# Performance work log

Measured on AMD Instinct MI355X. Metric: run time of the kernel, lower is better.

The kernel has to match this reference:

```python
import jax, jax.numpy as jnp
import numpy as np

HID = 128
HEADS = 4
CH = HID // HEADS          # 32
EDGE_DIM = 2 * HID         # H_update mode
GROUPS = 8
NEG_SLOPE = 0.2
EPS_GN = 1e-5
EPS_LN = 1e-5
N_NODES = 32768
N_EDGES = 524288


def setup_inputs() -> dict:
    key = jax.random.key(0)
    ks = jax.random.split(key, 32)
    N, E, C = N_NODES, N_EDGES, HID
    s = lambda fan: 1.0 / np.sqrt(fan)
    inp = dict(
        h_target=jax.random.normal(ks[0], (N, C), jnp.float32),
        h_source=jax.random.normal(ks[1], (N, C), jnp.float32),
        pos=jax.random.normal(ks[2], (N, 2), jnp.float32),
        t_emb=jax.random.normal(ks[3], (N, C), jnp.float32),
        edge_index=jax.random.randint(ks[4], (2, E), 0, N, jnp.int32),
        # AdaGN params
        gn_gamma=jnp.ones((C,), jnp.float32),
        gn_beta=jnp.zeros((C,), jnp.float32),
        fc_W=jax.random.normal(ks[5], (C, 2 * C), jnp.float32) * s(C),
        fc_b=jnp.zeros((2 * C,), jnp.float32),
        # GATv2 params
        Wl=jax.random.normal(ks[6], (C, HEADS * CH), jnp.float32) * s(C),
        bl=jnp.zeros((HEADS * CH,), jnp.float32),
        Wr=jax.random.normal(ks[7], (C, HEADS * CH), jnp.float32) * s(C),
        br=jnp.zeros((HEADS * CH,), jnp.float32),
        We=jax.random.normal(ks[8], (EDGE_DIM, HEADS * CH), jnp.float32) * s(EDGE_DIM),
        att=jax.random.normal(ks[9], (HEADS, CH), jnp.float32) * s(CH),
        gat_bias=jnp.zeros((HEADS * CH,), jnp.float32),
        # post GAT linear
        Wpost=jax.random.normal(ks[10], (C, C), jnp.float32) * s(C),
        bpost=jnp.zeros((C,), jnp.float32),
        # update MLP: LayerNorm -> Linear -> GELU -> Linear
        ln_g=jnp.ones((C,), jnp.float32),
        ln_b=jnp.zeros((C,), jnp.float32),
        W1=jax.random.normal(ks[11], (C, C), jnp.float32) * s(C),
        b1=jnp.zeros((C,), jnp.float32),
        W2=jax.random.normal(ks[12], (C, C), jnp.float32) * s(C),
        b2=jnp.zeros((C,), jnp.float32),
    )
    return inp


def _adagn(x, cond, gn_gamma, gn_beta, fc_W, fc_b):
    N, C = x.shape
    xg = x.reshape(N, GROUPS, C // GROUPS)
    mu = xg.mean(-1, keepdims=True)
    var = xg.var(-1, keepdims=True)
    normed = ((xg - mu) * jax.lax.rsqrt(var + EPS_GN)).reshape(N, C)
    normed = normed * gn_gamma + gn_beta
    style = cond @ fc_W + fc_b
    gamma, beta = jnp.split(style, 2, axis=-1)
    return normed * (1.0 + gamma) + beta


def reference(h_target, h_source, pos, t_emb, edge_index,
              gn_gamma, gn_beta, fc_W, fc_b,
              Wl, bl, Wr, br, We, att, gat_bias,
              Wpost, bpost, ln_g, ln_b, W1, b1, W2, b2):
    N, C = h_source.shape
    src, dst = edge_index[0], edge_index[1]

    h_src_mod = _adagn(h_source, t_emb, gn_gamma, gn_beta, fc_W, fc_b)

    # physics edge features (H_update mode)
    d_vec = pos[src] - pos[dst]                       # [E,2]
    dx, dy = d_vec[:, 0:1], d_vec[:, 1:2]
    dist_sq = jnp.maximum((d_vec ** 2).sum(-1, keepdims=True), 1e-8)
    grad_mag = (h_src_mod[src] - h_src_mod[dst]) / dist_sq   # [E,C]
    edge_attr = jnp.concatenate([grad_mag * (-dy), grad_mag * dx], axis=-1)  # [E,2C]

    # GATv2Conv (eval mode, no dropout)
    xl = (h_src_mod @ Wl + bl).reshape(N, HEADS, CH)  # source transform
    xr = (h_src_mod @ Wr + br).reshape(N, HEADS, CH)  # target transform
    e = (edge_attr @ We).reshape(-1, HEADS, CH)
    z = jax.nn.leaky_relu(xl[src] + xr[dst] + e, NEG_SLOPE)   # [E,H,Ch]
    logit = jnp.einsum('ehc,hc->eh', z, att)                  # [E,H]
    m = jax.ops.segment_max(logit, dst, num_segments=N)       # [N,H]
    m = jnp.where(jnp.isfinite(m), m, 0.0)
    ex = jnp.exp(logit - m[dst])
    denom = jax.ops.segment_sum(ex, dst, num_segments=N)      # [N,H]
    alpha = ex / (denom[dst] + 1e-16)                         # [E,H]
    msg = xl[src] * alpha[..., None]                          # [E,H,Ch]
    aggr = jax.ops.segment_sum(msg, dst, num_segments=N).reshape(N, HEADS * CH)
    aggr = aggr + gat_bias

    aggr = aggr @ Wpost + bpost

    # update MLP with residual
    mu = aggr.mean(-1, keepdims=True)
    var = aggr.var(-1, keepdims=True)
    ln = (aggr - mu) * jax.lax.rsqrt(var + EPS_LN) * ln_g + ln_b
    h = jax.nn.gelu(ln @ W1 + b1, approximate=False) @ W2 + b2
    return h_target + h
```

## Files before the change

### kernel.cpp

```cpp
#include <hip/hip_runtime.h>
#include <hip/hip_bf16.h>
#include <math.h>

#define HID 128

typedef __bf16 bf16x8 __attribute__((ext_vector_type(8)));
typedef float f32x4 __attribute__((ext_vector_type(4)));
union BF8 { uint4 u; bf16x8 v; unsigned short s[8]; };

__device__ __forceinline__ unsigned short f2bf(float x) {
  unsigned u = __float_as_uint(x);
  unsigned r = u + 0x7FFFu + ((u >> 16) & 1u);
  return (unsigned short)(r >> 16);
}
__device__ __forceinline__ float bf2f(unsigned short h) {
  return __uint_as_float(((unsigned)h) << 16);
}
__device__ __forceinline__ void ld2bf(const unsigned short* p, float& x, float& y) {
  unsigned v = *(const unsigned*)p;
  x = __uint_as_float((v & 0xFFFFu) << 16);
  y = __uint_as_float(v & 0xFFFF0000u);
}

__global__ void prep3(const float* __restrict__ fc_W, const float* __restrict__ Wl,
                      const float* __restrict__ Wr, const float* __restrict__ We,
                      const float* __restrict__ Wpost, const float* __restrict__ W1,
                      const float* __restrict__ W2, const float* __restrict__ bl,
                      const float* __restrict__ br, const float* __restrict__ gat_bias,
                      const float* __restrict__ bpost,
                      unsigned short* __restrict__ fcTh, unsigned short* __restrict__ fcTl,
                      unsigned short* __restrict__ WnTh, unsigned short* __restrict__ WnTl,
                      unsigned short* __restrict__ WpT, unsigned short* __restrict__ W1T,
                      unsigned short* __restrict__ W2T,
                      float* __restrict__ bxy, float* __restrict__ bpost2) {
  int gid = blockIdx.x * 256 + threadIdx.x;
  if (gid < 32768) {
    int n = gid >> 7, k = gid & 127;
    float x = fc_W[k * 256 + n];
    unsigned short h = f2bf(x);
    fcTh[n * 128 + k] = h;
    fcTl[n * 128 + k] = f2bf(x - bf2f(h));
  } else if (gid < 98304) {
    int i = gid - 32768; int n = i >> 7, k = i & 127;
    float x;
    if (n < 128)      x = Wl[k * 128 + n];
    else if (n < 256) x = Wr[k * 128 + (n - 128)];
    else if (n < 384) x = We[k * 128 + (n - 256)];
    else              x = We[(128 + k) * 128 + (n - 384)];
    unsigned short h = f2bf(x);
    WnTh[n * 128 + k] = h;
    if (n >= 256) WnTl[(n - 256) * 128 + k] = f2bf(x - bf2f(h));
  } else if (gid < 147456) {
    int i = gid - 98304; int which = i >> 14; int j = i & 16383;
    int n = j >> 7, k = j & 127;
    const float* W = (which == 0) ? Wpost : (which == 1) ? W1 : W2;
    unsigned short* T = (which == 0) ? WpT : (which == 1) ? W1T : W2T;
    T[n * 128 + k] = f2bf(W[k * 128 + n]);
  } else if (gid < 147712) {
    int j = gid - 147456;
    bxy[j] = (j < 128) ? bl[j] : br[j - 128];
  } else if (gid < 147840) {
    int t = gid - 147712;
    float s = bpost[t];
    for (int k = 0; k < 128; ++k) s += gat_bias[k] * Wpost[k * 128 + t];
    bpost2[t] = s;
  }
}

__global__ __launch_bounds__(256) void gemm_mfma(const float* __restrict__ A,
                                                 const unsigned short* __restrict__ WTh,
                                                 const unsigned short* __restrict__ WTl,
                                                 const float* __restrict__ bias,
                                                 float* __restrict__ C, int Ncols) {
  int tid = threadIdx.x;
  int wave = tid >> 6, lane = tid & 63;
  int m = lane & 15, q = lane >> 4;
  int r0 = blockIdx.x * 64 + wave * 16;
  const float* arow = A + (size_t)(r0 + m) * 128 + q * 8;
  BF8 Ah[4], Al[4];
#pragma unroll
  for (int kc = 0; kc < 4; ++kc) {
    float4 x0 = *(const float4*)(arow + kc * 32);
    float4 x1 = *(const float4*)(arow + kc * 32 + 4);
    float xs[8] = {x0.x, x0.y, x0.z, x0.w, x1.x, x1.y, x1.z, x1.w};
#pragma unroll
    for (int j = 0; j < 8; ++j) {
      unsigned short h = f2bf(xs[j]);
      Ah[kc].s[j] = h;
      Al[kc].s[j] = f2bf(xs[j] - bf2f(h));
    }
  }
  int ntiles = Ncols >> 4;
  for (int nt = 0; nt < ntiles; ++nt) {
    const unsigned short* wr  = WTh + (size_t)(nt * 16 + m) * 128 + q * 8;
    const unsigned short* wrl = WTl + (size_t)(nt * 16 + m) * 128 + q * 8;
    f32x4 acc = {0.f, 0.f, 0.f, 0.f};
#pragma unroll
    for (int kc = 0; kc < 4; ++kc) {
      BF8 bh, blo;
      bh.u  = *(const uint4*)(wr + kc * 32);
      blo.u = *(const uint4*)(wrl + kc * 32);
      acc = __builtin_amdgcn_mfma_f32_16x16x32_bf16(Ah[kc].v, bh.v, acc, 0, 0, 0);
      acc = __builtin_amdgcn_mfma_f32_16x16x32_bf16(Al[kc].v, bh.v, acc, 0, 0, 0);
      acc = __builtin_amdgcn_mfma_f32_16x16x32_bf16(Ah[kc].v, blo.v, acc, 0, 0, 0);
    }
    int n = nt * 16 + m;
    float bv = bias ? bias[n] : 0.0f;
#pragma unroll
    for (int i = 0; i < 4; ++i) {
      int row = r0 + q * 4 + i;
      C[(size_t)row * Ncols + n] = acc[i] + bv;
    }
  }
}

__global__ __launch_bounds__(256) void k_nodeP(const float* __restrict__ h_source,
                                               const float* __restrict__ style,
                                               const float* __restrict__ gn_gamma,
                                               const float* __restrict__ gn_beta,
                                               const unsigned short* __restrict__ WnTh,
                                               const unsigned short* __restrict__ WnTl,
                                               const float* __restrict__ bxy,
                                               unsigned short* __restrict__ packed,
                                               unsigned short* __restrict__ xrArr) {
  int tid = threadIdx.x, wave = tid >> 6, lane = tid & 63;
  int m = lane & 15, q = lane >> 4;
  int r0 = blockIdx.x * 128 + wave * 32;
  BF8 Ah[2][4], Al[2][4];
#pragma unroll
  for (int set = 0; set < 2; ++set) {
    int r = r0 + set * 16 + m;
    const float* hrow = h_source + (size_t)r * 128;
    const float* srow = style + (size_t)r * 256;
#pragma unroll
    for (int kc = 0; kc < 4; ++kc) {
      int ch = q * 8 + kc * 32;
      float4 x0 = *(const float4*)(hrow + ch);
      float4 x1 = *(const float4*)(hrow + ch + 4);
      float xs[8] = {x0.x, x0.y, x0.z, x0.w, x1.x, x1.y, x1.z, x1.w};
      float s8 = 0.f, q8 = 0.f;
#pragma unroll
      for (int j = 0; j < 8; ++j) { s8 += xs[j]; q8 += xs[j] * xs[j]; }
      float s16 = s8 + __shfl_xor(s8, 16);
      float q16 = q8 + __shfl_xor(q8, 16);
      float mu = s16 * (1.0f / 16.0f);
      float var = q16 * (1.0f / 16.0f) - mu * mu;
      float rv = rsqrtf(var + 1e-5f);
      float4 g0 = *(const float4*)(gn_gamma + ch);
      float4 g1 = *(const float4*)(gn_gamma + ch + 4);
      float4 be0 = *(const float4*)(gn_beta + ch);
      float4 be1 = *(const float4*)(gn_beta + ch + 4);
      float4 sg0 = *(const float4*)(srow + ch);
      float4 sg1 = *(const float4*)(srow + ch + 4);
      float4 sb0 = *(const float4*)(srow + 128 + ch);
      float4 sb1 = *(const float4*)(srow + 128 + ch + 4);
      float gg[8] = {g0.x, g0.y, g0.z, g0.w, g1.x, g1.y, g1.z, g1.w};
      float bb[8] = {be0.x, be0.y, be0.z, be0.w, be1.x, be1.y, be1.z, be1.w};
      float sg[8] = {sg0.x, sg0.y, sg0.z, sg0.w, sg1.x, sg1.y, sg1.z, sg1.w};
      float sb[8] = {sb0.x, sb0.y, sb0.z, sb0.w, sb1.x, sb1.y, sb1.z, sb1.w};
#pragma unroll
      for (int j = 0; j < 8; ++j) {
        float v = ((xs[j] - mu) * rv * gg[j] + bb[j]) * (1.0f + sg[j]) + sb[j];
        unsigned short h = f2bf(v);
        Ah[set][kc].s[j] = h;
        Al[set][kc].s[j] = f2bf(v - bf2f(h));
      }
    }
  }
  for (int nt = 0; nt < 32; ++nt) {
    f32x4 acc0 = {0.f, 0.f, 0.f, 0.f};
    f32x4 acc1 = {0.f, 0.f, 0.f, 0.f};
    const unsigned short* wr = WnTh + (size_t)(nt * 16 + m) * 128 + q * 8;
    if (nt < 16) {
#pragma unroll
      for (int kc = 0; kc < 4; ++kc) {
        BF8 bh; bh.u = *(const uint4*)(wr + kc * 32);
        acc0 = __builtin_amdgcn_mfma_f32_16x16x32_bf16(Ah[0][kc].v, bh.v, acc0, 0, 0, 0);
        acc1 = __builtin_amdgcn_mfma_f32_16x16x32_bf16(Ah[1][kc].v, bh.v, acc1, 0, 0, 0);
      }
    } else {
      const unsigned short* wl = WnTl + (size_t)((nt - 16) * 16 + m) * 128 + q * 8;
#pragma unroll
      for (int kc = 0; kc < 4; ++kc) {
        BF8 bh, blo;
        bh.u  = *(const uint4*)(wr + kc * 32);
        blo.u = *(const uint4*)(wl + kc * 32);
        acc0 = __builtin_amdgcn_mfma_f32_16x16x32_bf16(Ah[0][kc].v, bh.v, acc0, 0, 0, 0);
        acc0 = __builtin_amdgcn_mfma_f32_16x16x32_bf16(Al[0][kc].v, bh.v, acc0, 0, 0, 0);
        acc0 = __builtin_amdgcn_mfma_f32_16x16x32_bf16(Ah[0][kc].v, blo.v, acc0, 0, 0, 0);
        acc1 = __builtin_amdgcn_mfma_f32_16x16x32_bf16(Ah[1][kc].v, bh.v, acc1, 0, 0, 0);
        acc1 = __builtin_amdgcn_mfma_f32_16x16x32_bf16(Al[1][kc].v, bh.v, acc1, 0, 0, 0);
        acc1 = __builtin_amdgcn_mfma_f32_16x16x32_bf16(Ah[1][kc].v, blo.v, acc1, 0, 0, 0);
      }
    }
    int n = nt * 16 + m;
    float bv = (nt < 16) ? bxy[n] : 0.0f;
#pragma unroll
    for (int set = 0; set < 2; ++set) {
      f32x4 a = set ? acc1 : acc0;
#pragma unroll
      for (int i = 0; i < 4; ++i) {
        int row = r0 + set * 16 + q * 4 + i;
        unsigned short h = f2bf(a[i] + bv);
        if (nt < 8)       packed[(size_t)row * 384 + n] = h;
        else if (nt < 16) xrArr[(size_t)row * 128 + (n - 128)] = h;
        else              packed[(size_t)row * 384 + 128 + (n - 256)] = h;
      }
    }
  }
}

__global__ __launch_bounds__(256) void k_hist(const int* __restrict__ edst,
                                              int* __restrict__ count, int E) {
  int e = blockIdx.x * 256 + threadIdx.x;
  if (e < E) atomicAdd(&count[edst[e]], 1);
}

__global__ __launch_bounds__(1024) void k_scan(const int* __restrict__ count,
                                               int* __restrict__ rowptr,
                                               int* __restrict__ cursor, int N, int E) {
  __shared__ int part[1024];
  int t = threadIdx.x;
  int base = t * 32;
  int local[32];
  int s = 0;
#pragma unroll
  for (int i = 0; i < 32; ++i) { local[i] = count[base + i]; s += local[i]; }
  part[t] = s;
  __syncthreads();
  for (int off = 1; off < 1024; off <<= 1) {
    int v = part[t];
    int addv = (t >= off) ? part[t - off] : 0;
    __syncthreads();
    part[t] = v + addv;
    __syncthreads();
  }
  int run = (t == 0) ? 0 : part[t - 1];
#pragma unroll
  for (int i = 0; i < 32; ++i) {
    rowptr[base + i] = run;
    cursor[base + i] = run;
    run += local[i];
  }
  if (t == 1023) rowptr[N] = E;
}

__global__ __launch_bounds__(256) void k_scatter(const int* __restrict__ esrc,
                                                 const int* __restrict__ edst,
                                                 const float* __restrict__ pos,
                                                 int* __restrict__ cursor,
                                                 float4* __restrict__ meta, int E) {
  int e = blockIdx.x * 256 + threadIdx.x;
  if (e >= E) return;
  int src = esrc[e], dst = edst[e];
  int p = atomicAdd(&cursor[dst], 1);
  float2 ps = *(const float2*)(pos + 2 * src);
  float2 pd = *(const float2*)(pos + 2 * dst);
  float dx = ps.x - pd.x, dy = ps.y - pd.y;
  float d2 = fmaxf(dx * dx + dy * dy, 1e-8f);
  meta[p] = make_float4(__int_as_float(src), -dy / d2, dx / d2, 0.0f);
}

__device__ __forceinline__ void edge_step(float4 mt, const unsigned short* __restrict__ packed,
                                          int c0, float xr0, float xr1, float Ad0, float Ad1,
                                          float Bd0, float Bd1, float a0, float a1,
                                          float& m, float& l, float& s0, float& s1) {
  int s = __float_as_int(mt.x);
  float sy = mt.y, sx = mt.z;
  const unsigned short* pr = packed + (size_t)s * 384;
  float xl0, xl1, A0, A1, B0, B1;
  ld2bf(pr + c0, xl0, xl1);
  ld2bf(pr + 128 + c0, A0, A1);
  ld2bf(pr + 256 + c0, B0, B1);
  float z0 = xl0 + xr0 + sy * (A0 - Ad0) + sx * (B0 - Bd0);
  float z1 = xl1 + xr1 + sy * (A1 - Ad1) + sx * (B1 - Bd1);
  z0 = (z0 > 0.0f) ? z0 : 0.2f * z0;
  z1 = (z1 > 0.0f) ? z1 : 0.2f * z1;
  float p = a0 * z0 + a1 * z1;
#pragma unroll
  for (int mm = 8; mm >= 1; mm >>= 1) p += __shfl_xor(p, mm);
  float nm = fmaxf(m, p);
  float sc = expf(m - nm);
  float ex = expf(p - nm);
  l = l * sc + ex;
  s0 = s0 * sc + ex * xl0;
  s1 = s1 * sc + ex * xl1;
  m = nm;
}

__global__ __launch_bounds__(256) void k_edge(const int* __restrict__ rowptr,
                                              const float4* __restrict__ meta,
                                              const unsigned short* __restrict__ packed,
                                              const unsigned short* __restrict__ xrArr,
                                              const float* __restrict__ att,
                                              float* __restrict__ aggr, int N) {
  __shared__ float att_s[128];
  int tid = threadIdx.x;
  if (tid < 128) att_s[tid] = att[tid];
  __syncthreads();
  int d = blockIdx.x * 4 + (tid >> 6);
  if (d >= N) return;
  int lane = tid & 63;
  int c0 = lane * 2;
  float a0 = att_s[c0], a1 = att_s[c0 + 1];
  float xr0, xr1;
  ld2bf(xrArr + (size_t)d * 128 + c0, xr0, xr1);
  float Ad0, Ad1, Bd0, Bd1;
  ld2bf(packed + (size_t)d * 384 + 128 + c0, Ad0, Ad1);
  ld2bf(packed + (size_t)d * 384 + 256 + c0, Bd0, Bd1);

  int beg = rowptr[d], end = rowptr[d + 1];
  float m1 = -INFINITY, l1 = 0.f, p10 = 0.f, p11 = 0.f;
  float m2 = -INFINITY, l2 = 0.f, p20 = 0.f, p21 = 0.f;
  int j = beg;
  for (; j + 1 < end; j += 2) {
    float4 mta = meta[j];
    float4 mtb = meta[j + 1];
    edge_step(mta, packed, c0, xr0, xr1, Ad0, Ad1, Bd0, Bd1, a0, a1, m1, l1, p10, p11);
    edge_step(mtb, packed, c0, xr0, xr1, Ad0, Ad1, Bd0, Bd1, a0, a1, m2, l2, p20, p21);
  }
  if (j < end) {
    float4 mta = meta[j];
    edge_step(mta, packed, c0, xr0, xr1, Ad0, Ad1, Bd0, Bd1, a0, a1, m1, l1, p10, p11);
  }
  float nm = fmaxf(m1, m2);
  float sc1 = (m1 == nm) ? 1.0f : expf(m1 - nm);
  float sc2 = (m2 == nm) ? 1.0f : expf(m2 - nm);
  float l = l1 * sc1 + l2 * sc2;
  float o0 = p10 * sc1 + p20 * sc2;
  float o1 = p11 * sc1 + p21 * sc2;
  float inv = 1.0f / (l + 1e-16f);
  *(float2*)&aggr[(size_t)d * 128 + c0] = make_float2(o0 * inv, o1 * inv);
}

__global__ __launch_bounds__(256) void k_mlp(const float* __restrict__ aggr,
                                             const unsigned short* __restrict__ WpT,
                                             const unsigned short* __restrict__ W1T,
                                             const unsigned short* __restrict__ W2T,
                                             const float* __restrict__ bpost2,
                                             const float* __restrict__ b1,
                                             const float* __restrict__ b2,
                                             const float* __restrict__ ln_g,
                                             const float* __restrict__ ln_b,
                                             const float* __restrict__ h_target,
                                             float* __restrict__ out) {
  __shared__ unsigned short Tb[64 * 136];
  __shared__ unsigned short Ub[64 * 136];
  int tid = threadIdx.x, wave = tid >> 6, lane = tid & 63;
  int m = lane & 15, q = lane >> 4;
  int r0 = blockIdx.x * 64 + wave * 16;
  int rb0 = wave * 16;
  BF8 Af[4];
  {
    const float* arow = aggr + (size_t)(r0 + m) * 128 + q * 8;
#pragma unroll
    for (int kc = 0; kc < 4; ++kc) {
      float4 x0 = *(const float4*)(arow + kc * 32);
      float4 x1 = *(const float4*)(arow + kc * 32 + 4);
      float xs[8] = {x0.x, x0.y, x0.z, x0.w, x1.x, x1.y, x1.z, x1.w};
#pragma unroll
      for (int jj = 0; jj < 8; ++jj) Af[kc].s[jj] = f2bf(xs[jj]);
    }
  }
  f32x4 acc[8];
#pragma unroll
  for (int t = 0; t < 8; ++t) {
    const unsigned short* wr = WpT + (size_t)(t * 16 + m) * 128 + q * 8;
    f32x4 a = {0.f, 0.f, 0.f, 0.f};
#pragma unroll
    for (int kc = 0; kc < 4; ++kc) {
      BF8 bh; bh.u = *(const uint4*)(wr + kc * 32);
      a = __builtin_amdgcn_mfma_f32_16x16x32_bf16(Af[kc].v, bh.v, a, 0, 0, 0);
    }
    acc[t] = a;
  }
  float sum[4] = {0, 0, 0, 0}, sq[4] = {0, 0, 0, 0};
#pragma unroll
  for (int t = 0; t < 8; ++t) {
    float bv = bpost2[t * 16 + m];
#pragma unroll
    for (int i = 0; i < 4; ++i) {
      float v = acc[t][i] + bv;
      acc[t][i] = v;
      sum[i] += v;
      sq[i] += v * v;
    }
  }
#pragma unroll
  for (int i = 0; i < 4; ++i) {
#pragma unroll
    for (int w = 1; w <= 8; w <<= 1) {
      sum[i] += __shfl_xor(sum[i], w);
      sq[i] += __shfl_xor(sq[i], w);
    }
  }
  float mu[4], rv[4];
#pragma unroll
  for (int i = 0; i < 4; ++i) {
    mu[i] = sum[i] * (1.0f / 128.0f);
    float var = sq[i] * (1.0f / 128.0f) - mu[i] * mu[i];
    rv[i] = rsqrtf(var + 1e-5f);
  }
#pragma unroll
  for (int t = 0; t < 8; ++t) {
    int n = t * 16 + m;
    float g = ln_g[n], b = ln_b[n];
#pragma unroll
    for (int i = 0; i < 4; ++i) {
      float v = (acc[t][i] - mu[i]) * rv[i] * g + b;
      Tb[(rb0 + q * 4 + i) * 136 + n] = f2bf(v);
    }
  }
  __syncthreads();
  BF8 Bf[4];
  {
    const unsigned short* tp = Tb + (rb0 + m) * 136 + q * 8;
#pragma unroll
    for (int kc = 0; kc < 4; ++kc) Bf[kc].u = *(const uint4*)(tp + kc * 32);
  }
#pragma unroll
  for (int t = 0; t < 8; ++t) {
    const unsigned short* wr = W1T + (size_t)(t * 16 + m) * 128 + q * 8;
    f32x4 a = {0.f, 0.f, 0.f, 0.f};
#pragma unroll
    for (int kc = 0; kc < 4; ++kc) {
      BF8 bh; bh.u = *(const uint4*)(wr + kc * 32);
      a = __builtin_amdgcn_mfma_f32_16x16x32_bf16(Bf[kc].v, bh.v, a, 0, 0, 0);
    }
    acc[t] = a;
  }
#pragma unroll
  for (int t = 0; t < 8; ++t) {
    int n = t * 16 + m;
    float bv = b1[n];
#pragma unroll
    for (int i = 0; i < 4; ++i) {
      float v = acc[t][i] + bv;
      v = 0.5f * v * (1.0f + erff(v * 0.70710678118654752f));
      Ub[(rb0 + q * 4 + i) * 136 + n] = f2bf(v);
    }
  }
  __syncthreads();
  BF8 Cf[4];
  {
    const unsigned short* up = Ub + (rb0 + m) * 136 + q * 8;
#pragma unroll
    for (int kc = 0; kc < 4; ++kc) Cf[kc].u = *(const uint4*)(up + kc * 32);
  }
#pragma unroll
  for (int t = 0; t < 8; ++t) {
    const unsigned short* wr = W2T + (size_t)(t * 16 + m) * 128 + q * 8;
    f32x4 a = {0.f, 0.f, 0.f, 0.f};
#pragma unroll
    for (int kc = 0; kc < 4; ++kc) {
      BF8 bh; bh.u = *(const uint4*)(wr + kc * 32);
      a = __builtin_amdgcn_mfma_f32_16x16x32_bf16(Cf[kc].v, bh.v, a, 0, 0, 0);
    }
    int n = t * 16 + m;
    float bv = b2[n];
#pragma unroll
    for (int i = 0; i < 4; ++i) {
      size_t off = (size_t)(r0 + q * 4 + i) * 128 + n;
      out[off] = a[i] + bv + h_target[off];
    }
  }
}

extern "C" void kernel_launch(void* const* d_in, const int* in_sizes, int n_in,
                              void* d_out, int out_size, void* d_ws, size_t ws_size,
                              hipStream_t stream) {
  const float* h_target = (const float*)d_in[0];
  const float* h_source = (const float*)d_in[1];
  const float* pos      = (const float*)d_in[2];
  const float* t_emb    = (const float*)d_in[3];
  const int*   eidx     = (const int*)d_in[4];
  const float* gn_gamma = (const float*)d_in[5];
  const float* gn_beta  = (const float*)d_in[6];
  const float* fc_W     = (const float*)d_in[7];
  const float* fc_b     = (const float*)d_in[8];
  const float* Wl       = (const float*)d_in[9];
  const float* bl       = (const float*)d_in[10];
  const float* Wr       = (const float*)d_in[11];
  const float* br       = (const float*)d_in[12];
  const float* We       = (const float*)d_in[13];
  const float* att      = (const float*)d_in[14];
  const float* gat_bias = (const float*)d_in[15];
  const float* Wpost    = (const float*)d_in[16];
  const float* bpost    = (const float*)d_in[17];
  const float* ln_g     = (const float*)d_in[18];
  const float* ln_b     = (const float*)d_in[19];
  const float* W1       = (const float*)d_in[20];
  const float* b1       = (const float*)d_in[21];
  const float* W2       = (const float*)d_in[22];
  const float* b2       = (const float*)d_in[23];

  const int N = in_sizes[0] / HID;
  const int E = in_sizes[4] / 2;
  const int* esrc = eidx;
  const int* edst = eidx + E;

  float* ws = (float*)d_ws;
  const size_t MF = 1024 * 1024;
  float* style  = ws;
  float* aggr   = ws;
  unsigned short* packed = (unsigned short*)(ws + 8 * MF);
  unsigned short* xrArr  = (unsigned short*)(ws + 14 * MF);
  float4* meta  = (float4*)(ws + 16 * MF);
  int*   rowptr = (int*)(ws + 18 * MF);
  int*   count  = rowptr + 32832;
  int*   cursor = count + 32832;
  unsigned short* wgt = (unsigned short*)(ws + 18 * MF + 131072);
  unsigned short* fcTh = wgt;
  unsigned short* fcTl = wgt + 32768;
  unsigned short* WnTh = wgt + 65536;
  unsigned short* WnTl = wgt + 131072;
  unsigned short* WpT  = wgt + 163840;
  unsigned short* W1T  = wgt + 180224;
  unsigned short* W2T  = wgt + 196608;
  float* bxy    = (float*)(wgt + 212992);
  float* bpost2 = bxy + 256;
  const size_t needed = (size_t)(18 * MF + 131072 + 106496 + 512) * 4;
  if (ws_size < needed) return;

  dim3 blk(256);

  prep3<<<578, blk, 0, stream>>>(fc_W, Wl, Wr, We, Wpost, W1, W2, bl, br, gat_bias, bpost,
                                 fcTh, fcTl, WnTh, WnTl, WpT, W1T, W2T, bxy, bpost2);
  gemm_mfma<<<N / 64, blk, 0, stream>>>(t_emb, fcTh, fcTl, fc_b, style, 256);
  k_nodeP<<<N / 128, blk, 0, stream>>>(h_source, style, gn_gamma, gn_beta, WnTh, WnTl, bxy,
                                       packed, xrArr);
  hipMemsetAsync(count, 0, (size_t)N * 4, stream);
  k_hist<<<(E + 255) / 256, blk, 0, stream>>>(edst, count, E);
  k_scan<<<1, 1024, 0, stream>>>(count, rowptr, cursor, N, E);
  k_scatter<<<(E + 255) / 256, blk, 0, stream>>>(esrc, edst, pos, cursor, meta, E);
  k_edge<<<(N + 3) / 4, blk, 0, stream>>>(rowptr, meta, packed, xrArr, att, aggr, N);
  k_mlp<<<N / 64, blk, 0, stream>>>(aggr, WpT, W1T, W2T, bpost2, b1, b2, ln_g, ln_b,
                                    h_target, (float*)d_out);
}
```

Measured before the change: 374.3 us.

## Rewrite scan with wave shuffles and streamline edge softmax step

The single-block prefix scan drops its shared-memory Hillis-Steele loop, which needed many barriers, in favour of wave-level shuffle scans with int4 loads and stores. The edge kernel now uses nontemporal loads and stores for the edge metadata and reads packed bf16 pairs as 32-bit words. It also branches the online softmax so only one exp is evaluated per edge. The att vector is read directly from global memory instead of through shared memory. The branch can diverge across lanes, though all lanes in a 16-lane head group share the same p.

Measured after the change: 394.1 us. 1.05x slower.

```diff
diff --git a/kernel.cpp b/kernel.cpp
--- a/kernel.cpp
+++ b/kernel.cpp
@@ -6,6 +6,7 @@
 
 typedef __bf16 bf16x8 __attribute__((ext_vector_type(8)));
 typedef float f32x4 __attribute__((ext_vector_type(4)));
+typedef float nf4 __attribute__((ext_vector_type(4)));
 union BF8 { uint4 u; bf16x8 v; unsigned short s[8]; };
 
 __device__ __forceinline__ unsigned short f2bf(float x) {
@@ -20,6 +21,21 @@
   unsigned v = *(const unsigned*)p;
   x = __uint_as_float((v & 0xFFFFu) << 16);
   y = __uint_as_float(v & 0xFFFF0000u);
+}
+__device__ __forceinline__ float2 pk_add2(float2 a, float2 b) {
+  return make_float2(a.x + b.x, a.y + b.y);
+}
+__device__ __forceinline__ float2 pk_sub2(float2 a, float2 b) {
+  return make_float2(a.x - b.x, a.y - b.y);
+}
+__device__ __forceinline__ float2 pk_fma2(float2 a, float2 b, float2 c) {
+  return make_float2(fmaf(a.x, b.x, c.x), fmaf(a.y, b.y, c.y));
+}
+__device__ __forceinline__ float2 pk_max2(float2 a, float2 b) {
+  return make_float2(fmaxf(a.x, b.x), fmaxf(a.y, b.y));
+}
+__device__ __forceinline__ float2 pk_muls2(float2 a, float b) {
+  return make_float2(a.x * b, a.y * b);
 }
 
 __global__ void prep3(const float* __restrict__ fc_W, const float* __restrict__ Wl,
@@ -219,28 +235,47 @@
 __global__ __launch_bounds__(1024) void k_scan(const int* __restrict__ count,
                                                int* __restrict__ rowptr,
                                                int* __restrict__ cursor, int N, int E) {
-  __shared__ int part[1024];
+  __shared__ int wtot[16];
   int t = threadIdx.x;
-  int base = t * 32;
-  int local[32];
+  int lane = t & 63, wv = t >> 6;
+  int base4 = t * 8;
+  int4 L[8];
   int s = 0;
 #pragma unroll
-  for (int i = 0; i < 32; ++i) { local[i] = count[base + i]; s += local[i]; }
-  part[t] = s;
+  for (int i = 0; i < 8; ++i) {
+    L[i] = ((const int4*)count)[base4 + i];
+    s += L[i].x + L[i].y + L[i].z + L[i].w;
+  }
+  int incl = s;
+#pragma unroll
+  for (int off = 1; off < 64; off <<= 1) {
+    int v = __shfl_up(incl, off);
+    if (lane >= off) incl += v;
+  }
+  if (lane == 63) wtot[wv] = incl;
   __syncthreads();
-  for (int off = 1; off < 1024; off <<= 1) {
-    int v = part[t];
-    int addv = (t >= off) ? part[t - off] : 0;
-    __syncthreads();
-    part[t] = v + addv;
-    __syncthreads();
-  }
-  int run = (t == 0) ? 0 : part[t - 1];
-#pragma unroll
-  for (int i = 0; i < 32; ++i) {
-    rowptr[base + i] = run;
-    cursor[base + i] = run;
-    run += local[i];
+  if (t < 16) {
+    int v = wtot[t];
+    int sc = v;
+#pragma unroll
+    for (int off = 1; off < 16; off <<= 1) {
+      int u = __shfl_up(sc, off, 16);
+      if (t >= off) sc += u;
+    }
+    wtot[t] = sc - v;
+  }
+  __syncthreads();
+  int run = wtot[wv] + (incl - s);
+#pragma unroll
+  for (int i = 0; i < 8; ++i) {
+    int4 c = L[i];
+    int4 r;
+    r.x = run; run += c.x;
+    r.y = run; run += c.y;
+    r.z = run; run += c.z;
+    r.w = run; run += c.w;
+    ((int4*)rowptr)[base4 + i] = r;
+    ((int4*)cursor)[base4 + i] = r;
   }
   if (t == 1023) rowptr[N] = E;
 }
@@ -249,7 +284,7 @@
                                                  const int* __restrict__ edst,
                                                  const float* __restrict__ pos,
                                                  int* __restrict__ cursor,
-                                                 float4* __restrict__ meta, int E) {
+                                                 nf4* __restrict__ meta, int E) {
   int e = blockIdx.x * 256 + threadIdx.x;
   if (e >= E) return;
   int src = esrc[e], dst = edst[e];
@@ -258,77 +293,82 @@
   float2 pd = *(const float2*)(pos + 2 * dst);
   float dx = ps.x - pd.x, dy = ps.y - pd.y;
   float d2 = fmaxf(dx * dx + dy * dy, 1e-8f);
-  meta[p] = make_float4(__int_as_float(src), -dy / d2, dx / d2, 0.0f);
-}
-
-__device__ __forceinline__ void edge_step(float4 mt, const unsigned short* __restrict__ packed,
-                                          int c0, float xr0, float xr1, float Ad0, float Ad1,
-                                          float Bd0, float Bd1, float a0, float a1,
-                                          float& m, float& l, float& s0, float& s1) {
-  int s = __float_as_int(mt.x);
-  float sy = mt.y, sx = mt.z;
-  const unsigned short* pr = packed + (size_t)s * 384;
-  float xl0, xl1, A0, A1, B0, B1;
-  ld2bf(pr + c0, xl0, xl1);
-  ld2bf(pr + 128 + c0, A0, A1);
-  ld2bf(pr + 256 + c0, B0, B1);
-  float z0 = xl0 + xr0 + sy * (A0 - Ad0) + sx * (B0 - Bd0);
-  float z1 = xl1 + xr1 + sy * (A1 - Ad1) + sx * (B1 - Bd1);
-  z0 = (z0 > 0.0f) ? z0 : 0.2f * z0;
-  z1 = (z1 > 0.0f) ? z1 : 0.2f * z1;
-  float p = a0 * z0 + a1 * z1;
+  nf4 v = {__int_as_float(src), -dy / d2, dx / d2, 0.0f};
+  __builtin_nontemporal_store(v, &meta[p]);
+}
+
+__device__ __forceinline__ void edge_step(nf4 mt, const unsigned* __restrict__ packedW,
+                                          int lane, float2 xr, float2 Ad, float2 Bd,
+                                          float a0, float a1,
+                                          float& m, float& l, float2& s) {
+  int si = __float_as_int(mt.x);
+  const unsigned* pr = packedW + (size_t)si * 192;
+  unsigned wxl = pr[lane];
+  unsigned wA  = pr[64 + lane];
+  unsigned wB  = pr[128 + lane];
+  float2 xl = make_float2(__uint_as_float(wxl << 16), __uint_as_float(wxl & 0xFFFF0000u));
+  float2 A  = make_float2(__uint_as_float(wA << 16),  __uint_as_float(wA & 0xFFFF0000u));
+  float2 B  = make_float2(__uint_as_float(wB << 16),  __uint_as_float(wB & 0xFFFF0000u));
+  float2 z = pk_add2(xl, xr);
+  z = pk_fma2(make_float2(mt.y, mt.y), pk_sub2(A, Ad), z);
+  z = pk_fma2(make_float2(mt.z, mt.z), pk_sub2(B, Bd), z);
+  float2 zl = pk_max2(z, pk_muls2(z, 0.2f));
+  float p = fmaf(a0, zl.x, a1 * zl.y);
 #pragma unroll
   for (int mm = 8; mm >= 1; mm >>= 1) p += __shfl_xor(p, mm);
-  float nm = fmaxf(m, p);
-  float sc = expf(m - nm);
-  float ex = expf(p - nm);
-  l = l * sc + ex;
-  s0 = s0 * sc + ex * xl0;
-  s1 = s1 * sc + ex * xl1;
-  m = nm;
+  if (p <= m) {
+    float ex = expf(p - m);
+    l += ex;
+    s = pk_fma2(make_float2(ex, ex), xl, s);
+  } else {
+    float sc = expf(m - p);
+    l = fmaf(l, sc, 1.0f);
+    s = pk_fma2(make_float2(sc, sc), s, xl);
+    m = p;
+  }
 }
 
 __global__ __launch_bounds__(256) void k_edge(const int* __restrict__ rowptr,
-                                              const float4* __restrict__ meta,
+                                              const nf4* __restrict__ meta,
                                               const unsigned short* __restrict__ packed,
                                               const unsigned short* __restrict__ xrArr,
                                               const float* __restrict__ att,
                                               float* __restrict__ aggr, int N) {
-  __shared__ float att_s[128];
   int tid = threadIdx.x;
-  if (tid < 128) att_s[tid] = att[tid];
-  __syncthreads();
   int d = blockIdx.x * 4 + (tid >> 6);
   if (d >= N) return;
   int lane = tid & 63;
   int c0 = lane * 2;
-  float a0 = att_s[c0], a1 = att_s[c0 + 1];
-  float xr0, xr1;
-  ld2bf(xrArr + (size_t)d * 128 + c0, xr0, xr1);
-  float Ad0, Ad1, Bd0, Bd1;
-  ld2bf(packed + (size_t)d * 384 + 128 + c0, Ad0, Ad1);
-  ld2bf(packed + (size_t)d * 384 + 256 + c0, Bd0, Bd1);
-
+  float2 av = *(const float2*)(att + c0);
+  const unsigned* packedW = (const unsigned*)packed;
+  float2 xr, Ad, Bd;
+  ld2bf(xrArr + (size_t)d * 128 + c0, xr.x, xr.y);
+  {
+    const unsigned* pd = packedW + (size_t)d * 192;
+    unsigned wA = pd[64 + lane], wB = pd[128 + lane];
+    Ad = make_float2(__uint_as_float(wA << 16), __uint_as_float(wA & 0xFFFF0000u));
+    Bd = make_float2(__uint_as_float(wB << 16), __uint_as_float(wB & 0xFFFF0000u));
+  }
   int beg = rowptr[d], end = rowptr[d + 1];
-  float m1 = -INFINITY, l1 = 0.f, p10 = 0.f, p11 = 0.f;
-  float m2 = -INFINITY, l2 = 0.f, p20 = 0.f, p21 = 0.f;
+  float m1 = -INFINITY, l1 = 0.f; float2 s1 = make_float2(0.f, 0.f);
+  float m2 = -INFINITY, l2 = 0.f; float2 s2 = make_float2(0.f, 0.f);
   int j = beg;
   for (; j + 1 < end; j += 2) {
-    float4 mta = meta[j];
-    float4 mtb = meta[j + 1];
-    edge_step(mta, packed, c0, xr0, xr1, Ad0, Ad1, Bd0, Bd1, a0, a1, m1, l1, p10, p11);
-    edge_step(mtb, packed, c0, xr0, xr1, Ad0, Ad1, Bd0, Bd1, a0, a1, m2, l2, p20, p21);
+    nf4 mta = __builtin_nontemporal_load(&meta[j]);
+    nf4 mtb = __builtin_nontemporal_load(&meta[j + 1]);
+    edge_step(mta, packedW, lane, xr, Ad, Bd, av.x, av.y, m1, l1, s1);
+    edge_step(mtb, packedW, lane, xr, Ad, Bd, av.x, av.y, m2, l2, s2);
   }
   if (j < end) {
-    float4 mta = meta[j];
-    edge_step(mta, packed, c0, xr0, xr1, Ad0, Ad1, Bd0, Bd1, a0, a1, m1, l1, p10, p11);
+    nf4 mta = __builtin_nontemporal_load(&meta[j]);
+    edge_step(mta, packedW, lane, xr, Ad, Bd, av.x, av.y, m1, l1, s1);
   }
   float nm = fmaxf(m1, m2);
   float sc1 = (m1 == nm) ? 1.0f : expf(m1 - nm);
   float sc2 = (m2 == nm) ? 1.0f : expf(m2 - nm);
-  float l = l1 * sc1 + l2 * sc2;
-  float o0 = p10 * sc1 + p20 * sc2;
-  float o1 = p11 * sc1 + p21 * sc2;
+  float l = fmaf(l1, sc1, l2 * sc2);
+  float o0 = fmaf(s1.x, sc1, s2.x * sc2);
+  float o1 = fmaf(s1.y, sc1, s2.y * sc2);
   float inv = 1.0f / (l + 1e-16f);
   *(float2*)&aggr[(size_t)d * 128 + c0] = make_float2(o0 * inv, o1 * inv);
 }
@@ -505,7 +545,7 @@
   float* aggr   = ws;
   unsigned short* packed = (unsigned short*)(ws + 8 * MF);
   unsigned short* xrArr  = (unsigned short*)(ws + 14 * MF);
-  float4* meta  = (float4*)(ws + 16 * MF);
+  nf4*   meta   = (nf4*)(ws + 16 * MF);
   int*   rowptr = (int*)(ws + 18 * MF);
   int*   count  = rowptr + 32832;
   int*   cursor = count + 32832;
@@ -529,7 +569,7 @@
   gemm_mfma<<<N / 64, blk, 0, stream>>>(t_emb, fcTh, fcTl, fc_b, style, 256);
   k_nodeP<<<N / 128, blk, 0, stream>>>(h_source, style, gn_gamma, gn_beta, WnTh, WnTl, bxy,
                                        packed, xrArr);
-  hipMemsetAsync(count, 0, (size_t)N * 4, stream);
+  (void)hipMemsetAsync(count, 0, (size_t)N * 4, stream);
   k_hist<<<(E + 255) / 256, blk, 0, stream>>>(edst, count, E);
   k_scan<<<1, 1024, 0, stream>>>(count, rowptr, cursor, N, E);
   k_scatter<<<(E + 255) / 256, blk, 0, stream>>>(esrc, edst, pos, cursor, meta, E);
```
